# Optimization experiments

Hardware: AMD Instinct MI355X
Metric: run time of the kernel (lower is better)

## Reference

```python
import jax, jax.numpy as jnp
import numpy as np

H, W, CIN, COUT, B = 56, 56, 64, 64, 32
K = 3            # kernel_size
WIN = 15         # win_range
R = (WIN - 1) // 2


def _make_sample_idx():
    """Per-pixel fixed random sample locations within a WINxWIN window,
    mirroring Dconv_drop.__init__ (random.sample over valid window indices)."""
    rng = np.random.default_rng(0)
    ii = np.arange(H)[:, None, None]          # [H,1,1]
    jj = np.arange(W)[None, :, None]          # [1,W,1]
    lo_i = np.maximum(0, ii - R); hi_i = np.minimum(H - 1, ii + R)
    lo_j = np.maximum(0, jj - R); hi_j = np.minimum(W - 1, jj + R)
    ri = rng.integers(np.broadcast_to(lo_i, (H, W, K * K)),
                      np.broadcast_to(hi_i, (H, W, K * K)) + 1)
    rj = rng.integers(np.broadcast_to(lo_j, (H, W, K * K)),
                      np.broadcast_to(hi_j, (H, W, K * K)) + 1)
    return (ri * W + rj).astype(np.int32)    # [H,W,9] indices into H*W


def setup_inputs() -> dict:
    key = jax.random.key(0)
    k1, k2 = jax.random.split(key)
    x = jax.random.normal(k1, (B, CIN, H, W), dtype=jnp.float32)
    weight = jax.random.normal(k2, (COUT, CIN, K, K), dtype=jnp.float32) * 0.05
    sample_idx = jnp.asarray(_make_sample_idx())
    return {"x": x, "weight": weight, "sample_idx": sample_idx}


def reference(x, weight, sample_idx):
    # x: [B,C,H,W]; sample_idx: [H,W,9] flat indices into H*W.
    # Original: scatter gathered pixels into [B,C,3H,3W] grid, then
    # stride-3 kernel-3 conv => per-pixel contraction over the 9 samples.
    b, c, h, w = x.shape
    x_flat = x.reshape(b, c, h * w)
    gathered = x_flat[:, :, sample_idx]              # [B,C,H,W,9]
    w_flat = weight.reshape(weight.shape[0], c, K * K)  # [O,C,9]
    out = jnp.einsum('bchwk,ock->bohw', gathered, w_flat)
    return out
```

## Files before the change

### kernel.cpp

```cpp
#include <hip/hip_runtime.h>
#include <hip/hip_bf16.h>

#define HH 56
#define WW 56
#define CIN 64
#define COUT 64
#define BATCH 32
#define KK 9
#define HWP (HH*WW)
#define NS 18
#define NTILE 49
#define NBLK (NTILE*BATCH)
#define XT_OFF 73728
#define XSW 33

typedef __attribute__((ext_vector_type(8))) short short8;
typedef __attribute__((ext_vector_type(4))) float float4v;
typedef __attribute__((ext_vector_type(4))) unsigned int uint4v;

__device__ __forceinline__ unsigned short f2bf(float f) {
    union { float f; unsigned u; } v; v.f = f;
    unsigned r = v.u + 0x7FFFu + ((v.u >> 16) & 1u);
    return (unsigned short)(r >> 16);
}

__device__ __forceinline__ void prepack_elem(const float* __restrict__ w,
                                             unsigned short* __restrict__ apack,
                                             int e) {
    int j = e & 7;
    int l = (e >> 3) & 63;
    int ss = e >> 9;
    int mb = ss / 18;
    int s  = ss - mb * 18;
    int o = mb * 16 + (l & 15);
    int c = ((s & 1) << 5) + ((l >> 4) << 3) + j;
    int k = s >> 1;
    apack[e] = f2bf(w[(o * CIN + c) * KK + k]);
}

__global__ __launch_bounds__(256) void prep_kernel(
    const float* __restrict__ x, const float* __restrict__ w,
    unsigned int* __restrict__ xt, unsigned short* __restrict__ apack)
{
    int bid = blockIdx.x;
    int t   = threadIdx.x;
    if (bid < 3136) {
        int u   = bid * 256 + t;
        int c2q = u & 7;
        int hwb = u >> 3;
        int b   = hwb / HWP;
        int hw  = hwb - b * HWP;
        const float* xb = x + ((size_t)b * CIN + c2q * 8) * HWP + hw;
        uint4v o;
        #pragma unroll
        for (int i = 0; i < 4; ++i) {
            float f0 = xb[(size_t)(2 * i) * HWP];
            float f1 = xb[(size_t)(2 * i + 1) * HWP];
            o[i] = (unsigned)f2bf(f0) | ((unsigned)f2bf(f1) << 16);
        }
        *(uint4v*)(xt + (size_t)hwb * 32 + c2q * 4) = o;
    } else {
        prepack_elem(w, apack, (bid - 3136) * 256 + t);
    }
}

__global__ __launch_bounds__(256) void prep_weights_only(
    const float* __restrict__ w, unsigned short* __restrict__ apack)
{
    prepack_elem(w, apack, blockIdx.x * 256 + threadIdx.x);
}

__global__ __launch_bounds__(256, 2) void dconv_main(
    const unsigned int* __restrict__ xt, const int* __restrict__ sidx,
    const unsigned short* __restrict__ apack, float* __restrict__ out)
{
    __shared__ unsigned int xs[488 * 32];

    const int t    = threadIdx.x;
    const int lane = t & 63;
    const int wv   = t >> 6;
    const int mbp  = wv >> 1;
    const int ntp  = wv & 1;
    const int col  = lane & 15;
    const int krow = lane >> 4;

    int bid  = blockIdx.x;
    int orig = (bid & 7) * 196 + (bid >> 3);
    int b    = orig / NTILE;
    int bx   = orig - b * NTILE;
    int ti = bx / 7, tj = bx - (bx / 7) * 7;
    int r0 = ti * 8 - 7; if (r0 < 0) r0 = 0;
    int c0 = tj * 8 - 7; if (c0 < 0) c0 = 0;

    const unsigned int* xtb = xt + (size_t)b * HWP * 32;
    for (int grp = wv; grp < 61; grp += 4) {
        int ls  = grp * 8 + (lane >> 3);
        int lsr = ls / 22;
        int lsc = ls - lsr * 22;
        int si = r0 + lsr; if (si > HH - 1) si = HH - 1;
        int sj = c0 + lsc; if (sj > WW - 1) sj = WW - 1;
        const unsigned int* src =
            xtb + (size_t)(si * WW + sj) * 32 + (((lane & 7) ^ (lane >> 3)) << 2);
        __builtin_amdgcn_global_load_lds(
            (const __attribute__((address_space(1))) unsigned int*)src,
            (__attribute__((address_space(3))) unsigned int*)(xs + grp * 256),
            16, 0, 0);
    }

    int lb[2][KK];
    #pragma unroll
    for (int nn = 0; nn < 2; ++nn) {
        int p  = (ntp * 2 + nn) * 16 + col;
        int gi = ti * 8 + (p >> 3), gj = tj * 8 + (p & 7);
        const int* sp = sidx + (gi * WW + gj) * KK;
        #pragma unroll
        for (int k = 0; k < KK; ++k) {
            int g  = sp[k];
            int si = g / WW, sj = g - si * WW;
            int row = (si - r0) * 22 + (sj - c0);
            lb[nn][k] = row * 128 + ((krow ^ (row & 7)) << 4);
        }
    }

    short8 areg[2][NS];
    #pragma unroll
    for (int m = 0; m < 2; ++m) {
        const unsigned short* ap = apack + ((mbp * 2 + m) * NS) * 512 + lane * 8;
        #pragma unroll
        for (int s = 0; s < NS; ++s)
            areg[m][s] = *(const short8*)(ap + s * 512);
    }
    __syncthreads();

    float4v zero = {0.f, 0.f, 0.f, 0.f};
    float4v acc[2][2] = {{zero, zero}, {zero, zero}};
    const char* xsb = (const char*)xs;

    #pragma unroll
    for (int k = 0; k < KK; ++k) {
        #pragma unroll
        for (int nn = 0; nn < 2; ++nn) {
            int o0 = lb[nn][k];
            short8 bv0 = *(const short8*)(xsb + o0);
            short8 bv1 = *(const short8*)(xsb + (o0 ^ 64));
            acc[0][nn] = __builtin_amdgcn_mfma_f32_16x16x32_bf16(
                areg[0][2 * k], bv0, acc[0][nn], 0, 0, 0);
            acc[1][nn] = __builtin_amdgcn_mfma_f32_16x16x32_bf16(
                areg[1][2 * k], bv0, acc[1][nn], 0, 0, 0);
            acc[0][nn] = __builtin_amdgcn_mfma_f32_16x16x32_bf16(
                areg[0][2 * k + 1], bv1, acc[0][nn], 0, 0, 0);
            acc[1][nn] = __builtin_amdgcn_mfma_f32_16x16x32_bf16(
                areg[1][2 * k + 1], bv1, acc[1][nn], 0, 0, 0);
        }
    }

    float* ob = out + ((size_t)b * COUT + mbp * 32) * HWP;
    #pragma unroll
    for (int m = 0; m < 2; ++m) {
        #pragma unroll
        for (int nn = 0; nn < 2; ++nn) {
            int p = (ntp * 2 + nn) * 16 + col;
            int g = (ti * 8 + (p >> 3)) * WW + tj * 8 + (p & 7);
            #pragma unroll
            for (int r = 0; r < 4; ++r)
                ob[(m * 16 + krow * 4 + r) * HWP + g] = acc[m][nn][r];
        }
    }
}

__global__ __launch_bounds__(256, 2) void dconv_fb(
    const float* __restrict__ x, const int* __restrict__ sidx,
    const unsigned short* __restrict__ apack, float* __restrict__ out)
{
    __shared__ unsigned int xs[484 * XSW];

    const int t    = threadIdx.x;
    const int lane = t & 63;
    const int wv   = t >> 6;
    const int mbp  = wv >> 1;
    const int ntp  = wv & 1;
    const int col  = lane & 15;
    const int krow = lane >> 4;
    const int bx   = blockIdx.x;
    const int b    = blockIdx.y;
    const int ti = bx / 7, tj = bx - (bx / 7) * 7;
    int r0 = ti * 8 - 7; if (r0 < 0) r0 = 0;
    int r1 = ti * 8 + 14; if (r1 > HH - 1) r1 = HH - 1;
    int c0 = tj * 8 - 7; if (c0 < 0) c0 = 0;
    int c1 = tj * 8 + 14; if (c1 > WW - 1) c1 = WW - 1;

    int lb[2][KK];
    #pragma unroll
    for (int nn = 0; nn < 2; ++nn) {
        int p  = (ntp * 2 + nn) * 16 + col;
        int gi = ti * 8 + (p >> 3), gj = tj * 8 + (p & 7);
        const int* sp = sidx + (gi * WW + gj) * KK;
        #pragma unroll
        for (int k = 0; k < KK; ++k) {
            int g  = sp[k];
            int si = g / WW, sj = g - si * WW;
            lb[nn][k] = ((si - r0) * 22 + (sj - c0)) * (XSW * 4);
        }
    }

    short8 areg[2][NS];
    #pragma unroll
    for (int m = 0; m < 2; ++m) {
        const unsigned short* ap = apack + ((mbp * 2 + m) * NS) * 512 + lane * 8;
        #pragma unroll
        for (int s = 0; s < NS; ++s)
            areg[m][s] = *(const short8*)(ap + s * 512);
    }

    const float* xb = x + (size_t)b * CIN * HWP;
    for (int e = t; e < 32 * 512; e += 256) {
        int c2 = e >> 9, ls = e & 511;
        if (ls < 484) {
            int lsr = ls / 22;
            int si = r0 + lsr, sj = c0 + (ls - lsr * 22);
            if (si <= r1 && sj <= c1) {
                int g = si * WW + sj;
                float f0 = xb[(2 * c2) * HWP + g];
                float f1 = xb[(2 * c2 + 1) * HWP + g];
                xs[ls * XSW + c2] =
                    (unsigned)f2bf(f0) | ((unsigned)f2bf(f1) << 16);
            }
        }
    }
    __syncthreads();

    float4v zero = {0.f, 0.f, 0.f, 0.f};
    float4v acc[2][2] = {{zero, zero}, {zero, zero}};
    const char* xsb = (const char*)xs + krow * 16;

    #pragma unroll
    for (int k = 0; k < KK; ++k) {
        #pragma unroll
        for (int nn = 0; nn < 2; ++nn) {
            const char* ba = xsb + lb[nn][k];
            union { int i[4]; short8 s8; } b0, b1;
            #pragma unroll
            for (int w = 0; w < 4; ++w) {
                b0.i[w] = *(const int*)(ba + w * 4);
                b1.i[w] = *(const int*)(ba + 64 + w * 4);
            }
            acc[0][nn] = __builtin_amdgcn_mfma_f32_16x16x32_bf16(
                areg[0][2 * k], b0.s8, acc[0][nn], 0, 0, 0);
            acc[1][nn] = __builtin_amdgcn_mfma_f32_16x16x32_bf16(
                areg[1][2 * k], b0.s8, acc[1][nn], 0, 0, 0);
            acc[0][nn] = __builtin_amdgcn_mfma_f32_16x16x32_bf16(
                areg[0][2 * k + 1], b1.s8, acc[0][nn], 0, 0, 0);
            acc[1][nn] = __builtin_amdgcn_mfma_f32_16x16x32_bf16(
                areg[1][2 * k + 1], b1.s8, acc[1][nn], 0, 0, 0);
        }
    }

    float* ob = out + ((size_t)b * COUT + mbp * 32) * HWP;
    #pragma unroll
    for (int m = 0; m < 2; ++m) {
        #pragma unroll
        for (int nn = 0; nn < 2; ++nn) {
            int p = (ntp * 2 + nn) * 16 + col;
            int g = (ti * 8 + (p >> 3)) * WW + tj * 8 + (p & 7);
            #pragma unroll
            for (int r = 0; r < 4; ++r)
                ob[(m * 16 + krow * 4 + r) * HWP + g] = acc[m][nn][r];
        }
    }
}

extern "C" void kernel_launch(void* const* d_in, const int* in_sizes, int n_in,
                              void* d_out, int out_size, void* d_ws, size_t ws_size,
                              hipStream_t stream) {
    const float* x    = (const float*)d_in[0];
    const float* w    = (const float*)d_in[1];
    const int*   sidx = (const int*)d_in[2];
    float* out = (float*)d_out;
    unsigned short* apack = (unsigned short*)d_ws;
    unsigned int*   xt    = (unsigned int*)((char*)d_ws + XT_OFF);

    size_t need = (size_t)XT_OFF + (size_t)BATCH * HWP * 128;
    if (ws_size >= need) {
        prep_kernel<<<3280, 256, 0, stream>>>(x, w, xt, apack);
        dconv_main<<<NBLK, 256, 0, stream>>>(xt, sidx, apack, out);
    } else {
        prep_weights_only<<<144, 256, 0, stream>>>(w, apack);
        dim3 grid(NTILE, BATCH);
        dconv_fb<<<grid, 256, 0, stream>>>(x, sidx, apack, out);
    }
}
```

Before: 36.40 us.

## Split channel halves into two LDS passes and stream weights from memory

The LDS tile is halved by loading only 32 of the 64 input channels per pass, and the kernel now loops over two channel halves with a sync after each. Weight fragments are no longer held in 36 registers; they are loaded from global memory inside the k loop. The min-blocks launch bound is removed. The intent is to cut LDS use and register pressure so more blocks fit per CU. The cost is two serialized load/compute phases with extra barriers and repeated weight loads.

Result: faster. 33.94 us (-6.8%).

```diff
diff --git a/kernel.cpp b/kernel.cpp
--- a/kernel.cpp
+++ b/kernel.cpp
@@ -70,11 +70,11 @@
     prepack_elem(w, apack, blockIdx.x * 256 + threadIdx.x);
 }
 
-__global__ __launch_bounds__(256, 2) void dconv_main(
+__global__ __launch_bounds__(256) void dconv_main(
     const unsigned int* __restrict__ xt, const int* __restrict__ sidx,
     const unsigned short* __restrict__ apack, float* __restrict__ out)
 {
-    __shared__ unsigned int xs[488 * 32];
+    __shared__ unsigned int xs[496 * 16];
 
     const int t    = threadIdx.x;
     const int lane = t & 63;
@@ -93,19 +93,7 @@
     int c0 = tj * 8 - 7; if (c0 < 0) c0 = 0;
 
     const unsigned int* xtb = xt + (size_t)b * HWP * 32;
-    for (int grp = wv; grp < 61; grp += 4) {
-        int ls  = grp * 8 + (lane >> 3);
-        int lsr = ls / 22;
-        int lsc = ls - lsr * 22;
-        int si = r0 + lsr; if (si > HH - 1) si = HH - 1;
-        int sj = c0 + lsc; if (sj > WW - 1) sj = WW - 1;
-        const unsigned int* src =
-            xtb + (size_t)(si * WW + sj) * 32 + (((lane & 7) ^ (lane >> 3)) << 2);
-        __builtin_amdgcn_global_load_lds(
-            (const __attribute__((address_space(1))) unsigned int*)src,
-            (__attribute__((address_space(3))) unsigned int*)(xs + grp * 256),
-            16, 0, 0);
-    }
+
 
     int lb[2][KK];
     #pragma unroll
@@ -118,40 +106,49 @@
             int g  = sp[k];
             int si = g / WW, sj = g - si * WW;
             int row = (si - r0) * 22 + (sj - c0);
-            lb[nn][k] = row * 128 + ((krow ^ (row & 7)) << 4);
-        }
-    }
-
-    short8 areg[2][NS];
-    #pragma unroll
-    for (int m = 0; m < 2; ++m) {
-        const unsigned short* ap = apack + ((mbp * 2 + m) * NS) * 512 + lane * 8;
-        #pragma unroll
-        for (int s = 0; s < NS; ++s)
-            areg[m][s] = *(const short8*)(ap + s * 512);
-    }
-    __syncthreads();
+            lb[nn][k] = row * 64 + ((krow ^ (row & 3)) << 4);
+        }
+    }
+
+    const unsigned short* apW = apack + (size_t)(mbp * 2 * NS) * 512 + lane * 8;
 
     float4v zero = {0.f, 0.f, 0.f, 0.f};
     float4v acc[2][2] = {{zero, zero}, {zero, zero}};
     const char* xsb = (const char*)xs;
 
     #pragma unroll
-    for (int k = 0; k < KK; ++k) {
-        #pragma unroll
-        for (int nn = 0; nn < 2; ++nn) {
-            int o0 = lb[nn][k];
-            short8 bv0 = *(const short8*)(xsb + o0);
-            short8 bv1 = *(const short8*)(xsb + (o0 ^ 64));
-            acc[0][nn] = __builtin_amdgcn_mfma_f32_16x16x32_bf16(
-                areg[0][2 * k], bv0, acc[0][nn], 0, 0, 0);
-            acc[1][nn] = __builtin_amdgcn_mfma_f32_16x16x32_bf16(
-                areg[1][2 * k], bv0, acc[1][nn], 0, 0, 0);
-            acc[0][nn] = __builtin_amdgcn_mfma_f32_16x16x32_bf16(
-                areg[0][2 * k + 1], bv1, acc[0][nn], 0, 0, 0);
-            acc[1][nn] = __builtin_amdgcn_mfma_f32_16x16x32_bf16(
-                areg[1][2 * k + 1], bv1, acc[1][nn], 0, 0, 0);
-        }
+    for (int sh = 0; sh < 2; ++sh) {
+        for (int grp = wv; grp < 31; grp += 4) {
+            int row = grp * 16 + (lane >> 2);
+            int rc  = row < 483 ? row : 483;
+            int lsr = rc / 22;
+            int lsc = rc - lsr * 22;
+            int si = r0 + lsr; if (si > HH - 1) si = HH - 1;
+            int sj = c0 + lsc; if (sj > WW - 1) sj = WW - 1;
+            int q  = (lane & 3) ^ (rc & 3);
+            const unsigned int* src =
+                xtb + (size_t)(si * WW + sj) * 32 + sh * 16 + (q << 2);
+            __builtin_amdgcn_global_load_lds(
+                (const __attribute__((address_space(1))) unsigned int*)src,
+                (__attribute__((address_space(3))) unsigned int*)(xs + grp * 256),
+                16, 0, 0);
+        }
+        __syncthreads();
+
+        #pragma unroll
+        for (int k = 0; k < KK; ++k) {
+            short8 a0 = *(const short8*)(apW + (size_t)(2 * k + sh) * 512);
+            short8 a1 = *(const short8*)(apW + (size_t)(NS + 2 * k + sh) * 512);
+            #pragma unroll
+            for (int nn = 0; nn < 2; ++nn) {
+                short8 bv = *(const short8*)(xsb + lb[nn][k]);
+                acc[0][nn] = __builtin_amdgcn_mfma_f32_16x16x32_bf16(
+                    a0, bv, acc[0][nn], 0, 0, 0);
+                acc[1][nn] = __builtin_amdgcn_mfma_f32_16x16x32_bf16(
+                    a1, bv, acc[1][nn], 0, 0, 0);
+            }
+        }
+        __syncthreads();
     }
 
     float* ob = out + ((size_t)b * COUT + mbp * 32) * HWP;
```
